# Performance work log

Measured on AMD Instinct MI355X. Metric: run time of the kernel, lower is better.

The kernel has to match this reference:

```python
import jax, jax.numpy as jnp
import numpy as np

D_MODEL = 256; N_HEADS = 8; N_LEVELS = 4; N_POINTS = 4; D_FF = 2048
SHAPES = [(128, 128), (64, 64), (32, 32), (16, 16)]  # (H_l, W_l) per level
LV = sum(h * w for h, w in SHAPES)  # 21760
B = 8; NQ = 900
EPS = 1e-5


def layer_norm(x, s, b):
    m = x.mean(-1, keepdims=True)
    v = x.var(-1, keepdims=True)
    return (x - m) * jax.lax.rsqrt(v + EPS) * s + b


def mha(q, k, v, in_w, in_b, out_w, out_b):
    # torch nn.MultiheadAttention, batch_first, eval mode (no dropout)
    Bq, Lq, C = q.shape
    h = N_HEADS; d = C // h
    wq, wk, wv = jnp.split(in_w, 3, axis=0)
    bq, bk, bv = jnp.split(in_b, 3)
    qh = (q @ wq.T + bq).reshape(Bq, Lq, h, d)
    kh = (k @ wk.T + bk).reshape(Bq, -1, h, d)
    vh = (v @ wv.T + bv).reshape(Bq, -1, h, d)
    scale = jnp.asarray(1.0 / np.sqrt(d), q.dtype)
    attn = jax.nn.softmax(jnp.einsum('bqhd,bkhd->bhqk', qh, kh) * scale, axis=-1)
    o = jnp.einsum('bhqk,bkhd->bqhd', attn, vh).reshape(Bq, Lq, C)
    return o @ out_w.T + out_b


def deform_attn(query, ref, memory, spatial_shapes, val_w, val_b, off_w, off_b, aw_w, aw_b, co_w, co_b):
    # MSDeformAttn forward (eval): offsets/weights from query, bilinear sample value per level/point
    Bq, Lq, C = query.shape
    h, L, P = N_HEADS, N_LEVELS, N_POINTS
    dh = C // h
    value = (memory @ val_w.T + val_b).reshape(Bq, -1, h, dh)  # (B, Lv, h, dh)
    off = (query @ off_w.T + off_b).reshape(Bq, Lq, h, L, P, 2)
    aw = jax.nn.softmax((query @ aw_w.T + aw_b).reshape(Bq, Lq, h, L * P), axis=-1)
    aw = aw.reshape(Bq, Lq, h, L, P)
    # normalizer = (W_l, H_l) per level
    normalizer = spatial_shapes[:, ::-1].astype(query.dtype)
    loc = ref[:, :, None, :, None, :] + off / normalizer[None, None, None, :, None, :]  # (B,Lq,h,L,P,2)
    out = jnp.zeros((Bq, h, Lq, dh), query.dtype)
    start = 0
    for l, (Hl, Wl) in enumerate(SHAPES):
        v_l = value[:, start:start + Hl * Wl].transpose(0, 2, 1, 3)  # (B,h,Hl*Wl,dh)
        start += Hl * Wl
        xy = loc[:, :, :, l]  # (B,Lq,h,P,2) normalized in [0,1]
        # grid_sample align_corners=False pixel coords
        x = xy[..., 0] * Wl - 0.5
        y = xy[..., 1] * Hl - 0.5
        x0 = jnp.floor(x); y0 = jnp.floor(y)
        wx = x - x0; wy = y - y0
        acc = jnp.zeros((Bq, h, Lq * P, dh), query.dtype)
        for dx, dy, w in ((0, 0, (1 - wx) * (1 - wy)), (1, 0, wx * (1 - wy)),
                          (0, 1, (1 - wx) * wy), (1, 1, wx * wy)):
            xi = x0 + dx; yi = y0 + dy
            valid = (xi >= 0) & (xi <= Wl - 1) & (yi >= 0) & (yi <= Hl - 1)
            xi = jnp.clip(xi, 0, Wl - 1).astype(jnp.int32)
            yi = jnp.clip(yi, 0, Hl - 1).astype(jnp.int32)
            idx = (yi * Wl + xi).transpose(0, 2, 1, 3).reshape(Bq, h, Lq * P)
            g = jnp.take_along_axis(v_l, idx[..., None], axis=2)  # (B,h,Lq*P,dh)
            wgt = (w * valid).transpose(0, 2, 1, 3).reshape(Bq, h, Lq * P)
            acc = acc + g * wgt[..., None]
        acc = acc.reshape(Bq, h, Lq, P, dh)
        wl = aw[:, :, :, l].transpose(0, 2, 1, 3)  # (B,h,Lq,P)
        out = out + jnp.einsum('bhqpd,bhqp->bhqd', acc, wl)
    out = out.transpose(0, 2, 1, 3).reshape(Bq, Lq, C)
    return out @ co_w.T + co_b


def forward(tgt, memory, query_pos, reference_points, sa_in_w, sa_in_b, sa_out_w, sa_out_b,
            off_w, off_b, aw_w, aw_b, val_w, val_b, co_w, co_b,
            l1_w, l1_b, l2_w, l2_b, ln1_s, ln1_b, ln2_s, ln2_b, ln3_s, ln3_b, spatial_shapes):
    q = tgt + query_pos  # with_pos_embed; eval mode: no group_detr split, no dropout
    tgt2 = mha(q, q, tgt, sa_in_w, sa_in_b, sa_out_w, sa_out_b)
    tgt = layer_norm(tgt + tgt2, ln1_s, ln1_b)
    tgt2 = deform_attn(tgt + query_pos, reference_points, memory, spatial_shapes,
                       val_w, val_b, off_w, off_b, aw_w, aw_b, co_w, co_b)
    tgt = layer_norm(tgt + tgt2, ln2_s, ln2_b)
    tgt2 = jax.nn.relu(tgt @ l1_w.T + l1_b) @ l2_w.T + l2_b
    return layer_norm(tgt + tgt2, ln3_s, ln3_b)


def setup_inputs():
    key = jax.random.key(0)
    ks = jax.random.split(key, 16)
    C = D_MODEL
    f = lambda i, shape, s=0.02: jax.random.normal(ks[i], shape, jnp.float32) * s
    HLP = N_HEADS * N_LEVELS * N_POINTS
    return {
        'tgt': f(0, (B, NQ, C), 1.0),
        'memory': f(1, (B, LV, C), 1.0),
        'query_pos': f(2, (B, NQ, C), 1.0),
        'reference_points': jax.random.uniform(ks[3], (B, NQ, N_LEVELS, 2), jnp.float32),
        'sa_in_w': f(4, (3 * C, C)), 'sa_in_b': jnp.zeros((3 * C,), jnp.float32),
        'sa_out_w': f(5, (C, C)), 'sa_out_b': jnp.zeros((C,), jnp.float32),
        'off_w': f(6, (HLP * 2, C)), 'off_b': f(7, (HLP * 2,), 0.5),
        'aw_w': f(8, (HLP, C)), 'aw_b': jnp.zeros((HLP,), jnp.float32),
        'val_w': f(9, (C, C)), 'val_b': jnp.zeros((C,), jnp.float32),
        'co_w': f(10, (C, C)), 'co_b': jnp.zeros((C,), jnp.float32),
        'l1_w': f(11, (D_FF, C)), 'l1_b': jnp.zeros((D_FF,), jnp.float32),
        'l2_w': f(12, (C, D_FF)), 'l2_b': jnp.zeros((C,), jnp.float32),
        'ln1_s': jnp.ones((C,), jnp.float32), 'ln1_b': jnp.zeros((C,), jnp.float32),
        'ln2_s': jnp.ones((C,), jnp.float32), 'ln2_b': jnp.zeros((C,), jnp.float32),
        'ln3_s': jnp.ones((C,), jnp.float32), 'ln3_b': jnp.zeros((C,), jnp.float32),
        'spatial_shapes': jnp.asarray(SHAPES, jnp.int32),
        'level_start_index': jnp.asarray(np.cumsum([0] + [h * w for h, w in SHAPES[:-1]]), jnp.int32),
    }


def reference(tgt, memory, query_pos, reference_points, sa_in_w, sa_in_b, sa_out_w, sa_out_b,
              off_w, off_b, aw_w, aw_b, val_w, val_b, co_w, co_b,
              l1_w, l1_b, l2_w, l2_b, ln1_s, ln1_b, ln2_s, ln2_b, ln3_s, ln3_b,
              spatial_shapes, level_start_index):
    return forward(tgt, memory, query_pos, reference_points, sa_in_w, sa_in_b, sa_out_w, sa_out_b,
                   off_w, off_b, aw_w, aw_b, val_w, val_b, co_w, co_b,
                   l1_w, l1_b, l2_w, l2_b, ln1_s, ln1_b, ln2_s, ln2_b, ln3_s, ln3_b, spatial_shapes)
```

## Files before the change

### kernel.cpp

```cpp
#include <hip/hip_runtime.h>
#include <hip/hip_bf16.h>

#define NQL 900
#define CDIM 256
#define BDIM 8
#define LVTOT 21760

typedef __bf16 bf16x8 __attribute__((ext_vector_type(8)));
typedef float f32x4 __attribute__((ext_vector_type(4)));
typedef uint u32x4 __attribute__((ext_vector_type(4)));
typedef uint u32x2 __attribute__((ext_vector_type(2)));

__device__ __forceinline__ ushort f2bf(float x) {
  uint u = __builtin_bit_cast(uint, x);
  u += 0x7fff + ((u >> 16) & 1);
  return (ushort)(u >> 16);
}

template <bool ABF16, bool AADD, bool RELU, bool OUTBF16>
__global__ __launch_bounds__(256, 4) void mgemm_kernel(const void* __restrict__ Ap,
                                                       const float* __restrict__ A2p,
                                                       const float* __restrict__ W,
                                                       const float* __restrict__ bias,
                                                       void* __restrict__ Cout,
                                                       int M, int N, int K) {
  __shared__ ushort smem[10240];
  ushort* As = smem;
  ushort* Bs = smem + 5120;
  const int tid = threadIdx.x;
  const int m0 = blockIdx.y * 128, n0 = blockIdx.x * 128;
  const int wv = tid >> 6;
  const int wm = (wv >> 1) * 64, wn = (wv & 1) * 64;
  const int lane = tid & 63;
  const int lr = lane & 15, kq = lane >> 4;

  f32x4 acc[4][4] = {};
  float4 pa[2][2], pb[2][2];
  u32x4 pa16[2];

  auto load_tiles = [&](int k0) {
#pragma unroll
    for (int it = 0; it < 2; ++it) {
      int idx = it * 256 + tid;
      int r = idx >> 2, s = (idx & 3) << 3;
      int gm = min(m0 + r, M - 1);
      if constexpr (ABF16) {
        pa16[it] = *(const u32x4*)((const ushort*)Ap + (size_t)gm * K + k0 + s);
      } else {
        const float* ap = (const float*)Ap + (size_t)gm * K + k0 + s;
        pa[it][0] = *(const float4*)ap;
        pa[it][1] = *(const float4*)(ap + 4);
        if constexpr (AADD) {
          const float* ap2 = A2p + (size_t)gm * K + k0 + s;
          float4 q0 = *(const float4*)ap2;
          float4 q1 = *(const float4*)(ap2 + 4);
          pa[it][0].x += q0.x; pa[it][0].y += q0.y; pa[it][0].z += q0.z; pa[it][0].w += q0.w;
          pa[it][1].x += q1.x; pa[it][1].y += q1.y; pa[it][1].z += q1.z; pa[it][1].w += q1.w;
        }
      }
      int gn = min(n0 + r, N - 1);
      const float* wp = W + (size_t)gn * K + k0 + s;
      pb[it][0] = *(const float4*)wp;
      pb[it][1] = *(const float4*)(wp + 4);
    }
  };

  auto store_tiles = [&]() {
#pragma unroll
    for (int it = 0; it < 2; ++it) {
      int idx = it * 256 + tid;
      int r = idx >> 2, s = (idx & 3) << 3;
      u32x4 u;
      if constexpr (ABF16) {
        u = pa16[it];
      } else {
        u.x = f2bf(pa[it][0].x) | ((uint)f2bf(pa[it][0].y) << 16);
        u.y = f2bf(pa[it][0].z) | ((uint)f2bf(pa[it][0].w) << 16);
        u.z = f2bf(pa[it][1].x) | ((uint)f2bf(pa[it][1].y) << 16);
        u.w = f2bf(pa[it][1].z) | ((uint)f2bf(pa[it][1].w) << 16);
      }
      *(u32x4*)&As[r * 40 + s] = u;
      u32x4 w;
      w.x = f2bf(pb[it][0].x) | ((uint)f2bf(pb[it][0].y) << 16);
      w.y = f2bf(pb[it][0].z) | ((uint)f2bf(pb[it][0].w) << 16);
      w.z = f2bf(pb[it][1].x) | ((uint)f2bf(pb[it][1].y) << 16);
      w.w = f2bf(pb[it][1].z) | ((uint)f2bf(pb[it][1].w) << 16);
      *(u32x4*)&Bs[r * 40 + s] = w;
    }
  };

  load_tiles(0);
  for (int k0 = 0; k0 < K; k0 += 32) {
    store_tiles();
    __syncthreads();
    if (k0 + 32 < K) load_tiles(k0 + 32);
    bf16x8 af[4], bq[4];
#pragma unroll
    for (int m = 0; m < 4; ++m)
      af[m] = __builtin_bit_cast(bf16x8, *(const u32x4*)&As[(wm + m * 16 + lr) * 40 + kq * 8]);
#pragma unroll
    for (int n = 0; n < 4; ++n)
      bq[n] = __builtin_bit_cast(bf16x8, *(const u32x4*)&Bs[(wn + n * 16 + lr) * 40 + kq * 8]);
#pragma unroll
    for (int m = 0; m < 4; ++m)
#pragma unroll
      for (int n = 0; n < 4; ++n)
        acc[m][n] = __builtin_amdgcn_mfma_f32_16x16x32_bf16(af[m], bq[n], acc[m][n], 0, 0, 0);
    __syncthreads();
  }

  if constexpr (OUTBF16) {
    ushort* Cs = smem;
#pragma unroll
    for (int p = 0; p < 2; ++p) {
      __syncthreads();
      if (wm == p * 64) {
#pragma unroll
        for (int n = 0; n < 4; ++n) {
          int col = wn + n * 16 + lr;
          float bv = bias[n0 + col];
#pragma unroll
          for (int m = 0; m < 4; ++m)
#pragma unroll
            for (int j = 0; j < 4; ++j) {
              float v = acc[m][n][j] + bv;
              if (RELU) v = fmaxf(v, 0.f);
              Cs[(m * 16 + kq * 4 + j) * 136 + col] = f2bf(v);
            }
        }
      }
      __syncthreads();
#pragma unroll
      for (int it = 0; it < 4; ++it) {
        int idx = it * 256 + tid;
        int r = idx >> 4, c = (idx & 15) * 8;
        int grow = m0 + p * 64 + r;
        if (grow < M) {
          u32x4 u = *(const u32x4*)&Cs[r * 136 + c];
          *(u32x4*)((ushort*)Cout + (size_t)grow * N + n0 + c) = u;
        }
      }
    }
  } else {
#pragma unroll
    for (int n = 0; n < 4; ++n) {
      int gcol = n0 + wn + n * 16 + lr;
      float bv = bias[gcol];
#pragma unroll
      for (int m = 0; m < 4; ++m) {
        int rbase = m0 + wm + m * 16 + kq * 4;
#pragma unroll
        for (int j = 0; j < 4; ++j) {
          int grow = rbase + j;
          if (grow >= M) continue;
          float v = acc[m][n][j] + bv;
          if (RELU) v = fmaxf(v, 0.f);
          ((float*)Cout)[(size_t)grow * N + gcol] = v;
        }
      }
    }
  }
}

template <bool ABF16, bool AADD, bool RELU, bool HASRES, bool DOSM, bool OUTBF16>
__global__ __launch_bounds__(256, 4) void mgemm64_kernel(const void* __restrict__ Ap,
                                                         const float* __restrict__ A2p,
                                                         const float* __restrict__ W,
                                                         const float* __restrict__ bias,
                                                         const float* __restrict__ Rres,
                                                         void* __restrict__ Cout,
                                                         int M, int N, int K) {
  __shared__ ushort smem[5120];
  ushort* As = smem;
  ushort* Bs = smem + 2560;
  const int tid = threadIdx.x;
  const int m0 = blockIdx.y * 64, n0 = blockIdx.x * 64;
  const int wv = tid >> 6, lane = tid & 63;
  const int wm = (wv >> 1) * 32, wn = (wv & 1) * 32;
  const int lr = lane & 15, kq = lane >> 4;

  f32x4 acc[2][2] = {};
  float4 pa[2], pb[2];
  u32x4 pa16;

  auto load_tiles = [&](int k0) {
    int r = tid >> 2, s = (tid & 3) << 3;
    int gm = min(m0 + r, M - 1);
    if constexpr (ABF16) {
      pa16 = *(const u32x4*)((const ushort*)Ap + (size_t)gm * K + k0 + s);
    } else {
      const float* ap = (const float*)Ap + (size_t)gm * K + k0 + s;
      pa[0] = *(const float4*)ap;
      pa[1] = *(const float4*)(ap + 4);
      if constexpr (AADD) {
        const float* ap2 = A2p + (size_t)gm * K + k0 + s;
        float4 q0 = *(const float4*)ap2;
        float4 q1 = *(const float4*)(ap2 + 4);
        pa[0].x += q0.x; pa[0].y += q0.y; pa[0].z += q0.z; pa[0].w += q0.w;
        pa[1].x += q1.x; pa[1].y += q1.y; pa[1].z += q1.z; pa[1].w += q1.w;
      }
    }
    int gn = min(n0 + r, N - 1);
    const float* wp = W + (size_t)gn * K + k0 + s;
    pb[0] = *(const float4*)wp;
    pb[1] = *(const float4*)(wp + 4);
  };

  auto store_tiles = [&]() {
    int r = tid >> 2, s = (tid & 3) << 3;
    u32x4 u;
    if constexpr (ABF16) {
      u = pa16;
    } else {
      u.x = f2bf(pa[0].x) | ((uint)f2bf(pa[0].y) << 16);
      u.y = f2bf(pa[0].z) | ((uint)f2bf(pa[0].w) << 16);
      u.z = f2bf(pa[1].x) | ((uint)f2bf(pa[1].y) << 16);
      u.w = f2bf(pa[1].z) | ((uint)f2bf(pa[1].w) << 16);
    }
    *(u32x4*)&As[r * 40 + s] = u;
    u32x4 w;
    w.x = f2bf(pb[0].x) | ((uint)f2bf(pb[0].y) << 16);
    w.y = f2bf(pb[0].z) | ((uint)f2bf(pb[0].w) << 16);
    w.z = f2bf(pb[1].x) | ((uint)f2bf(pb[1].y) << 16);
    w.w = f2bf(pb[1].z) | ((uint)f2bf(pb[1].w) << 16);
    *(u32x4*)&Bs[r * 40 + s] = w;
  };

  load_tiles(0);
  for (int k0 = 0; k0 < K; k0 += 32) {
    store_tiles();
    __syncthreads();
    if (k0 + 32 < K) load_tiles(k0 + 32);
    bf16x8 af[2], bq[2];
#pragma unroll
    for (int m = 0; m < 2; ++m)
      af[m] = __builtin_bit_cast(bf16x8, *(const u32x4*)&As[(wm + m * 16 + lr) * 40 + kq * 8]);
#pragma unroll
    for (int n = 0; n < 2; ++n)
      bq[n] = __builtin_bit_cast(bf16x8, *(const u32x4*)&Bs[(wn + n * 16 + lr) * 40 + kq * 8]);
#pragma unroll
    for (int m = 0; m < 2; ++m)
#pragma unroll
      for (int n = 0; n < 2; ++n)
        acc[m][n] = __builtin_amdgcn_mfma_f32_16x16x32_bf16(af[m], bq[n], acc[m][n], 0, 0, 0);
    __syncthreads();
  }

  if constexpr (OUTBF16) {
    ushort* Cs = smem;
    __syncthreads();
#pragma unroll
    for (int n = 0; n < 2; ++n) {
      int col = wn + n * 16 + lr;
      float bv = bias[n0 + col];
#pragma unroll
      for (int m = 0; m < 2; ++m)
#pragma unroll
        for (int j = 0; j < 4; ++j) {
          float v = acc[m][n][j] + bv;
          if (RELU) v = fmaxf(v, 0.f);
          Cs[(wm + m * 16 + kq * 4 + j) * 72 + col] = f2bf(v);
        }
    }
    __syncthreads();
#pragma unroll
    for (int it = 0; it < 2; ++it) {
      int idx = it * 256 + tid;
      int r = idx >> 3, c = (idx & 7) * 8;
      int grow = m0 + r;
      if (grow < M) {
        u32x4 u = *(const u32x4*)&Cs[r * 72 + c];
        *(u32x4*)((ushort*)Cout + (size_t)grow * N + n0 + c) = u;
      }
    }
  } else {
#pragma unroll
    for (int n = 0; n < 2; ++n) {
      int gcol = n0 + wn + n * 16 + lr;
      float bv = bias[gcol];
#pragma unroll
      for (int m = 0; m < 2; ++m) {
        int rbase = m0 + wm + m * 16 + kq * 4;
#pragma unroll
        for (int j = 0; j < 4; ++j) {
          int grow = rbase + j;
          float v = acc[m][n][j] + bv;
          if constexpr (DOSM) {
            float gmax = v;
#pragma unroll
            for (int w = 1; w < 16; w <<= 1) gmax = fmaxf(gmax, __shfl_xor(gmax, w));
            float e = __expf(v - gmax);
            float gs = e;
#pragma unroll
            for (int w = 1; w < 16; w <<= 1) gs += __shfl_xor(gs, w);
            v = e / gs;
          }
          if (grow >= M) continue;
          if (HASRES) v += Rres[(size_t)grow * N + gcol];
          if (RELU) v = fmaxf(v, 0.f);
          ((float*)Cout)[(size_t)grow * N + gcol] = v;
        }
      }
    }
  }
}

template <bool ABF16, bool OUTBF16>
__global__ __launch_bounds__(256, 4) void mgemm256_kernel(const void* __restrict__ Ap,
                                                          const float* __restrict__ W,
                                                          const float* __restrict__ bias,
                                                          void* __restrict__ Cout,
                                                          int M, int K) {
  __shared__ ushort smem[12800];
  ushort* As = smem;
  ushort* Bs = smem + 2560;
  const int tid = threadIdx.x;
  const int m0 = blockIdx.x * 64;
  const int wv = tid >> 6;
  const int lane = tid & 63;
  const int lr = lane & 15, kq = lane >> 4;

  f32x4 acc[16] = {};
  float4 pa[2];
  u32x4 pa16;
  float4 pb[4][2];

  auto load_tiles = [&](int k0) {
    {
      int r = tid >> 2, s = (tid & 3) << 3;
      int gm = min(m0 + r, M - 1);
      if constexpr (ABF16) {
        pa16 = *(const u32x4*)((const ushort*)Ap + (size_t)gm * K + k0 + s);
      } else {
        const float* ap = (const float*)Ap + (size_t)gm * K + k0 + s;
        pa[0] = *(const float4*)ap;
        pa[1] = *(const float4*)(ap + 4);
      }
    }
#pragma unroll
    for (int it = 0; it < 4; ++it) {
      int idx = it * 256 + tid;
      int r = idx >> 2, s = (idx & 3) << 3;
      const float* wp = W + (size_t)r * K + k0 + s;
      pb[it][0] = *(const float4*)wp;
      pb[it][1] = *(const float4*)(wp + 4);
    }
  };

  auto store_tiles = [&]() {
    {
      int r = tid >> 2, s = (tid & 3) << 3;
      u32x4 u;
      if constexpr (ABF16) {
        u = pa16;
      } else {
        u.x = f2bf(pa[0].x) | ((uint)f2bf(pa[0].y) << 16);
        u.y = f2bf(pa[0].z) | ((uint)f2bf(pa[0].w) << 16);
        u.z = f2bf(pa[1].x) | ((uint)f2bf(pa[1].y) << 16);
        u.w = f2bf(pa[1].z) | ((uint)f2bf(pa[1].w) << 16);
      }
      *(u32x4*)&As[r * 40 + s] = u;
    }
#pragma unroll
    for (int it = 0; it < 4; ++it) {
      int idx = it * 256 + tid;
      int r = idx >> 2, s = (idx & 3) << 3;
      u32x4 w;
      w.x = f2bf(pb[it][0].x) | ((uint)f2bf(pb[it][0].y) << 16);
      w.y = f2bf(pb[it][0].z) | ((uint)f2bf(pb[it][0].w) << 16);
      w.z = f2bf(pb[it][1].x) | ((uint)f2bf(pb[it][1].y) << 16);
      w.w = f2bf(pb[it][1].z) | ((uint)f2bf(pb[it][1].w) << 16);
      *(u32x4*)&Bs[r * 40 + s] = w;
    }
  };

  load_tiles(0);
  for (int k0 = 0; k0 < K; k0 += 32) {
    store_tiles();
    __syncthreads();
    if (k0 + 32 < K) load_tiles(k0 + 32);
    bf16x8 af = __builtin_bit_cast(bf16x8, *(const u32x4*)&As[(wv * 16 + lr) * 40 + kq * 8]);
#pragma unroll
    for (int ng = 0; ng < 16; ++ng) {
      bf16x8 bq = __builtin_bit_cast(bf16x8, *(const u32x4*)&Bs[(ng * 16 + lr) * 40 + kq * 8]);
      acc[ng] = __builtin_amdgcn_mfma_f32_16x16x32_bf16(af, bq, acc[ng], 0, 0, 0);
    }
    __syncthreads();
  }

  if constexpr (OUTBF16) {
    ushort* Cs = smem;
#pragma unroll
    for (int p = 0; p < 2; ++p) {
      __syncthreads();
      if ((wv >> 1) == p) {
#pragma unroll
        for (int nf = 0; nf < 16; ++nf) {
          int col = nf * 16 + lr;
          float bv = bias[col];
#pragma unroll
          for (int j = 0; j < 4; ++j) {
            int row = (wv & 1) * 16 + kq * 4 + j;
            Cs[row * 264 + col] = f2bf(acc[nf][j] + bv);
          }
        }
      }
      __syncthreads();
#pragma unroll
      for (int it = 0; it < 4; ++it) {
        int idx = it * 256 + tid;
        int r = idx >> 5, c = (idx & 31) * 8;
        int grow = m0 + p * 32 + r;
        if (grow < M) {
          u32x4 u = *(const u32x4*)&Cs[r * 264 + c];
          *(u32x4*)((ushort*)Cout + (size_t)grow * 256 + c) = u;
        }
      }
    }
  } else {
#pragma unroll
    for (int nf = 0; nf < 16; ++nf) {
      int col = nf * 16 + lr;
      float bv = bias[col];
#pragma unroll
      for (int j = 0; j < 4; ++j) {
        int grow = m0 + wv * 16 + kq * 4 + j;
        if (grow < M)
          ((float*)Cout)[(size_t)grow * 256 + col] = acc[nf][j] + bv;
      }
    }
  }
}

__global__ __launch_bounds__(256) void vt_kernel(const ushort* __restrict__ tmp_v,
                                                 ushort* __restrict__ vt) {
  __shared__ ushort Ls[64 * 40];
  const int qt = blockIdx.x;
  const int bh = blockIdx.y;
  const int b = bh >> 3, h = bh & 7;
  const int tid = threadIdx.x;
  const int q0 = qt * 64;
  {
    int r = tid >> 2, c = (tid & 3) * 8;
    int gq = min(q0 + r, NQL - 1);
    u32x4 u = *(const u32x4*)(tmp_v + ((size_t)(b * NQL + gq) * 256) + h * 32 + c);
    *(u32x4*)&Ls[r * 40 + c] = u;
  }
  __syncthreads();
  {
    int d = tid >> 3, qw = (tid & 7) * 8;
    u32x4 u;
    uint w[8];
#pragma unroll
    for (int j = 0; j < 8; ++j) w[j] = Ls[(qw + j) * 40 + d];
    u.x = w[0] | (w[1] << 16);
    u.y = w[2] | (w[3] << 16);
    u.z = w[4] | (w[5] << 16);
    u.w = w[6] | (w[7] << 16);
    *(u32x4*)(vt + ((size_t)(bh * 32 + d) * 960) + q0 + qw) = u;
  }
}

__global__ __launch_bounds__(256, 2) void fattn_kernel(const ushort* __restrict__ qk,
                                                       const ushort* __restrict__ vt,
                                                       float* __restrict__ out) {
  __shared__ ushort Ks[64 * 40];
  __shared__ ushort Vs[32 * 72];
  __shared__ ushort Ps[4][16 * 72];
  const int qt = blockIdx.x, bh = blockIdx.y;
  const int b = bh >> 3, h = bh & 7;
  const int tid = threadIdx.x;
  const int wv = tid >> 6, lane = tid & 63;
  const int lq = lane & 15, hi = lane >> 4;
  const int q0 = qt * 64 + wv * 16;
  const float SC = 0.17677669529663689f;

  bf16x8 qfrag;
  {
    int qrow = min(q0 + lq, NQL - 1);
    qfrag = __builtin_bit_cast(bf16x8,
        *(const u32x4*)(qk + (size_t)(b * NQL + qrow) * 512 + h * 32 + hi * 8));
  }

  f32x4 o0 = {}, o1 = {};
  float mrow = -1e30f, lrow = 0.f;

  for (int kt = 0; kt < 15; ++kt) {
    const int k0 = kt * 64;
    __syncthreads();
    {
      int r = tid >> 2, c = (tid & 3) * 8;
      int gk = min(k0 + r, NQL - 1);
      u32x4 u = *(const u32x4*)(qk + (size_t)(b * NQL + gk) * 512 + 256 + h * 32 + c);
      *(u32x4*)&Ks[r * 40 + c] = u;
    }
    {
      int r = tid >> 3, c = (tid & 7) * 8;
      u32x4 u = *(const u32x4*)(vt + (size_t)(bh * 32 + r) * 960 + k0 + c);
      *(u32x4*)&Vs[r * 72 + c] = u;
    }
    __syncthreads();

    f32x4 st[4];
#pragma unroll
    for (int mt = 0; mt < 4; ++mt) {
      bf16x8 kf = __builtin_bit_cast(bf16x8, *(const u32x4*)&Ks[(mt * 16 + lq) * 40 + hi * 8]);
      f32x4 z = {};
      st[mt] = __builtin_amdgcn_mfma_f32_16x16x32_bf16(kf, qfrag, z, 0, 0, 0);
    }
    float sv[4][4];
    float lmax = -1e30f;
#pragma unroll
    for (int mt = 0; mt < 4; ++mt)
#pragma unroll
      for (int j = 0; j < 4; ++j) {
        int key = k0 + mt * 16 + hi * 4 + j;
        float v = st[mt][j] * SC;
        v = (key < NQL) ? v : -1e30f;
        sv[mt][j] = v;
        lmax = fmaxf(lmax, v);
      }
    lmax = fmaxf(lmax, __shfl_xor(lmax, 16));
    lmax = fmaxf(lmax, __shfl_xor(lmax, 32));
    float mnew = fmaxf(mrow, lmax);
    float rs = __expf(mrow - mnew);
    float lsum = 0.f;
    uint pw[4][2];
#pragma unroll
    for (int mt = 0; mt < 4; ++mt) {
      float p0 = __expf(sv[mt][0] - mnew);
      float p1 = __expf(sv[mt][1] - mnew);
      float p2 = __expf(sv[mt][2] - mnew);
      float p3 = __expf(sv[mt][3] - mnew);
      lsum += (p0 + p1) + (p2 + p3);
      pw[mt][0] = f2bf(p0) | ((uint)f2bf(p1) << 16);
      pw[mt][1] = f2bf(p2) | ((uint)f2bf(p3) << 16);
    }
    lsum += __shfl_xor(lsum, 16);
    lsum += __shfl_xor(lsum, 32);
    lrow = lrow * rs + lsum;
    mrow = mnew;
#pragma unroll
    for (int j = 0; j < 4; ++j) {
      float rsj = __shfl(rs, hi * 4 + j);
      o0[j] *= rsj;
      o1[j] *= rsj;
    }
#pragma unroll
    for (int mt = 0; mt < 4; ++mt) {
      u32x2 u;
      u.x = pw[mt][0];
      u.y = pw[mt][1];
      *(u32x2*)&Ps[wv][lq * 72 + mt * 16 + hi * 4] = u;
    }
#pragma unroll
    for (int k2 = 0; k2 < 2; ++k2) {
      bf16x8 pa = __builtin_bit_cast(bf16x8, *(const u32x4*)&Ps[wv][lq * 72 + k2 * 32 + hi * 8]);
      bf16x8 vb0 = __builtin_bit_cast(bf16x8, *(const u32x4*)&Vs[(0 * 16 + lq) * 72 + k2 * 32 + hi * 8]);
      bf16x8 vb1 = __builtin_bit_cast(bf16x8, *(const u32x4*)&Vs[(1 * 16 + lq) * 72 + k2 * 32 + hi * 8]);
      o0 = __builtin_amdgcn_mfma_f32_16x16x32_bf16(pa, vb0, o0, 0, 0, 0);
      o1 = __builtin_amdgcn_mfma_f32_16x16x32_bf16(pa, vb1, o1, 0, 0, 0);
    }
  }

#pragma unroll
  for (int j = 0; j < 4; ++j) {
    float lj = __shfl(lrow, hi * 4 + j);
    float inv = 1.f / lj;
    int gq = q0 + hi * 4 + j;
    if (gq < NQL) {
      float* op = out + (size_t)(b * NQL + gq) * 256 + h * 32;
      op[lq] = o0[j] * inv;
      op[16 + lq] = o1[j] * inv;
    }
  }
}

__global__ __launch_bounds__(256) void ln_kernel(const float* __restrict__ x,
                                                 const float* __restrict__ s,
                                                 const float* __restrict__ bb,
                                                 float* __restrict__ out, int M) {
  const int wv = threadIdx.x >> 6, lane = threadIdx.x & 63;
  const int row = blockIdx.x * 4 + wv;
  if (row >= M) return;
  const float4 v = *(const float4*)(x + (size_t)row * 256 + lane * 4);
  float s1 = (v.x + v.y) + (v.z + v.w);
  float s2 = (v.x * v.x + v.y * v.y) + (v.z * v.z + v.w * v.w);
#pragma unroll
  for (int w = 1; w < 64; w <<= 1) {
    s1 += __shfl_xor(s1, w);
    s2 += __shfl_xor(s2, w);
  }
  float mean = s1 * (1.f / 256.f);
  float var = s2 * (1.f / 256.f) - mean * mean;
  float inv = rsqrtf(var + 1e-5f);
  float4 sc = *(const float4*)(s + lane * 4);
  float4 bv = *(const float4*)(bb + lane * 4);
  float4 o;
  o.x = (v.x - mean) * inv * sc.x + bv.x;
  o.y = (v.y - mean) * inv * sc.y + bv.y;
  o.z = (v.z - mean) * inv * sc.z + bv.z;
  o.w = (v.w - mean) * inv * sc.w + bv.w;
  *(float4*)(out + (size_t)row * 256 + lane * 4) = o;
}

__global__ __launch_bounds__(256) void deform_kernel(const __hip_bfloat16* __restrict__ value,
                                                     const float* __restrict__ offb,
                                                     const float* __restrict__ awb,
                                                     const float* __restrict__ refp,
                                                     float* __restrict__ dfout) {
  const int Hs[4] = {128, 64, 32, 16};
  const int Stl[4] = {0, 16384, 20480, 21504};
  int row = blockIdx.x;
  int b = row / NQL;
  int tid = threadIdx.x;
  int h = tid >> 5, d = tid & 31;
  const float* off = offb + (size_t)row * 256;
  const float* aw = awb + (size_t)row * 128;
  const float* ref = refp + (size_t)row * 8;
  const __hip_bfloat16* vb = value + (size_t)b * LVTOT * 256 + h * 32 + d;
  float acc = 0.f;
#pragma unroll
  for (int l = 0; l < 4; ++l) {
    int Wi = Hs[l], Hi = Hs[l];
    float Wl = (float)Wi, Hl = (float)Hi;
    int st = Stl[l];
    float rx = ref[l * 2 + 0], ry = ref[l * 2 + 1];
#pragma unroll
    for (int p = 0; p < 4; ++p) {
      int oi = ((h * 4 + l) * 4 + p) * 2;
      float x = (rx + off[oi] / Wl) * Wl - 0.5f;
      float y = (ry + off[oi + 1] / Hl) * Hl - 0.5f;
      float w = aw[h * 16 + l * 4 + p];
      float x0f = floorf(x), y0f = floorf(y);
      float wx = x - x0f, wy = y - y0f;
      int xi0 = (int)x0f, yi0 = (int)y0f;
      float samp = 0.f;
#pragma unroll
      for (int dy = 0; dy < 2; ++dy) {
#pragma unroll
        for (int dx = 0; dx < 2; ++dx) {
          int xi = xi0 + dx, yi = yi0 + dy;
          float tw = (dx ? wx : 1.f - wx) * (dy ? wy : 1.f - wy);
          bool valid = (xi >= 0) && (xi < Wi) && (yi >= 0) && (yi < Hi);
          int xc = min(max(xi, 0), Wi - 1);
          int yc = min(max(yi, 0), Hi - 1);
          float vv = __bfloat162float(vb[(size_t)(st + yc * Wi + xc) * 256]);
          samp += valid ? tw * vv : 0.f;
        }
      }
      acc = fmaf(w, samp, acc);
    }
  }
  dfout[(size_t)row * 256 + tid] = acc;
}

extern "C" void kernel_launch(void* const* d_in, const int* in_sizes, int n_in,
                              void* d_out, int out_size, void* d_ws, size_t ws_size,
                              hipStream_t stream) {
  const float* tgt = (const float*)d_in[0];
  const float* memory = (const float*)d_in[1];
  const float* qpos = (const float*)d_in[2];
  const float* refp = (const float*)d_in[3];
  const float* sa_in_w = (const float*)d_in[4];
  const float* sa_in_b = (const float*)d_in[5];
  const float* sa_out_w = (const float*)d_in[6];
  const float* sa_out_b = (const float*)d_in[7];
  const float* off_w = (const float*)d_in[8];
  const float* off_b = (const float*)d_in[9];
  const float* aw_w = (const float*)d_in[10];
  const float* aw_b = (const float*)d_in[11];
  const float* val_w = (const float*)d_in[12];
  const float* val_b = (const float*)d_in[13];
  const float* co_w = (const float*)d_in[14];
  const float* co_b = (const float*)d_in[15];
  const float* l1_w = (const float*)d_in[16];
  const float* l1_b = (const float*)d_in[17];
  const float* l2_w = (const float*)d_in[18];
  const float* l2_b = (const float*)d_in[19];
  const float* ln1_s = (const float*)d_in[20];
  const float* ln1_b = (const float*)d_in[21];
  const float* ln2_s = (const float*)d_in[22];
  const float* ln2_b = (const float*)d_in[23];
  const float* ln3_s = (const float*)d_in[24];
  const float* ln3_b = (const float*)d_in[25];

  float* ws = (float*)d_ws;
  const size_t E = (size_t)BDIM * NQL * CDIM;
  ushort* vt = (ushort*)(ws + E);
  float* attn_o = ws + 4 * E;
  ushort* tmp_qk = (ushort*)(ws + 5 * E);
  ushort* tmp_v = (ushort*)(ws + 7 * E);
  float* sa_out = ws + 5 * E;
  float* offb = ws + E;
  float* awb = ws + 2 * E;
  float* dfout = ws + 3 * E;
  float* co_out = ws + 4 * E;
  ushort* hidden = (ushort*)ws;
  float* ffn_o = ws + 4 * E;
  float* tgt1 = ws + 8 * E;
  float* tgt2 = ws + 9 * E;
  ushort* valbf = (ushort*)(ws + 11 * E);

  const int M = BDIM * NQL;
  const int MT = (M + 127) / 128;
  const int M64 = (M + 63) / 64;
  const int LNG = (M + 3) / 4;
  dim3 blk(256);

  mgemm64_kernel<false, true, false, false, false, true><<<dim3(8, M64), blk, 0, stream>>>(
      tgt, qpos, sa_in_w, sa_in_b, nullptr, tmp_qk, M, 512, 256);
  mgemm64_kernel<false, false, false, false, false, true><<<dim3(4, M64), blk, 0, stream>>>(
      tgt, nullptr, sa_in_w + 512 * 256, sa_in_b + 512, nullptr, tmp_v, M, 256, 256);
  vt_kernel<<<dim3(15, 64), blk, 0, stream>>>(tmp_v, vt);
  fattn_kernel<<<dim3(15, 64), blk, 0, stream>>>(tmp_qk, vt, attn_o);
  mgemm64_kernel<false, false, false, true, false, false><<<dim3(4, M64), blk, 0, stream>>>(
      attn_o, nullptr, sa_out_w, sa_out_b, tgt, sa_out, M, 256, 256);
  ln_kernel<<<LNG, blk, 0, stream>>>(sa_out, ln1_s, ln1_b, tgt1, M);
  mgemm256_kernel<false, true><<<(BDIM * LVTOT) / 64, blk, 0, stream>>>(
      memory, val_w, val_b, valbf, BDIM * LVTOT, 256);
  mgemm64_kernel<false, true, false, false, false, false><<<dim3(4, M64), blk, 0, stream>>>(
      tgt1, qpos, off_w, off_b, nullptr, offb, M, 256, 256);
  mgemm64_kernel<false, true, false, false, true, false><<<dim3(2, M64), blk, 0, stream>>>(
      tgt1, qpos, aw_w, aw_b, nullptr, awb, M, 128, 256);
  deform_kernel<<<M, blk, 0, stream>>>((const __hip_bfloat16*)valbf, offb, awb, refp, dfout);
  mgemm64_kernel<false, false, false, true, false, false><<<dim3(4, M64), blk, 0, stream>>>(
      dfout, nullptr, co_w, co_b, tgt1, co_out, M, 256, 256);
  ln_kernel<<<LNG, blk, 0, stream>>>(co_out, ln2_s, ln2_b, tgt2, M);
  mgemm_kernel<false, false, true, true><<<dim3(16, MT), blk, 0, stream>>>(
      tgt2, nullptr, l1_w, l1_b, hidden, M, 2048, 256);
  mgemm64_kernel<true, false, false, true, false, false><<<dim3(4, M64), blk, 0, stream>>>(
      hidden, nullptr, l2_w, l2_b, tgt2, ffn_o, M, 256, 2048);
  ln_kernel<<<LNG, blk, 0, stream>>>(ffn_o, ln3_s, ln3_b, (float*)d_out, M);
}
```

Measured before the change: 359.4 us.

## Pre-convert value weights to bf16 and stage full A row-tile in LDS

Adds a small kernel that converts the value-projection weight to bf16 once per call, and rewrites the value projection GEMM to load the whole 64x256 fp32 memory tile up front into LDS as bf16. Per k-step it now only streams pre-converted bf16 weights instead of reloading and converting fp32 weights in every block. This removes the repeated per-block fp32-to-bf16 conversion of W and halves weight traffic. The cost is a larger LDS footprint (lower occupancy, launch bounds 2) and one extra small launch.

Result: no change. 357.3 us (-0.6%).

```diff
diff --git a/kernel.cpp b/kernel.cpp
--- a/kernel.cpp
+++ b/kernel.cpp
@@ -305,81 +305,65 @@
   }
 }
 
-template <bool ABF16, bool OUTBF16>
-__global__ __launch_bounds__(256, 4) void mgemm256_kernel(const void* __restrict__ Ap,
-                                                          const float* __restrict__ W,
-                                                          const float* __restrict__ bias,
-                                                          void* __restrict__ Cout,
-                                                          int M, int K) {
-  __shared__ ushort smem[12800];
-  ushort* As = smem;
-  ushort* Bs = smem + 2560;
+__global__ __launch_bounds__(256) void wconv_kernel(const float* __restrict__ W,
+                                                    ushort* __restrict__ Wbf) {
+  int idx = (blockIdx.x * 256 + threadIdx.x) * 4;
+  float4 v = *(const float4*)(W + idx);
+  u32x2 u;
+  u.x = f2bf(v.x) | ((uint)f2bf(v.y) << 16);
+  u.y = f2bf(v.z) | ((uint)f2bf(v.w) << 16);
+  *(u32x2*)(Wbf + idx) = u;
+}
+
+__global__ __launch_bounds__(256, 2) void vproj_kernel(const float* __restrict__ A,
+                                                       const ushort* __restrict__ Wbf,
+                                                       const float* __restrict__ bias,
+                                                       ushort* __restrict__ Cout) {
+  __shared__ ushort As[64 * 264];
+  __shared__ ushort Bs[256 * 40];
   const int tid = threadIdx.x;
   const int m0 = blockIdx.x * 64;
-  const int wv = tid >> 6;
-  const int lane = tid & 63;
+  const int wv = tid >> 6, lane = tid & 63;
   const int lr = lane & 15, kq = lane >> 4;
 
+  {
+    const float* base = A + (size_t)m0 * 256;
+    float4 v[16];
+#pragma unroll
+    for (int it = 0; it < 16; ++it)
+      v[it] = *(const float4*)(base + (size_t)(it * 256 + tid) * 4);
+#pragma unroll
+    for (int it = 0; it < 16; ++it) {
+      int f4 = it * 256 + tid;
+      int row = f4 >> 6;
+      int col = (f4 & 63) * 4;
+      u32x2 w;
+      w.x = f2bf(v[it].x) | ((uint)f2bf(v[it].y) << 16);
+      w.y = f2bf(v[it].z) | ((uint)f2bf(v[it].w) << 16);
+      *(u32x2*)&As[row * 264 + col] = w;
+    }
+  }
+
+  u32x4 pw[4];
+  auto loadW = [&](int k0) {
+#pragma unroll
+    for (int i = 0; i < 4; ++i)
+      pw[i] = *(const u32x4*)(Wbf + (size_t)tid * 256 + k0 + i * 8);
+  };
+  auto storeW = [&]() {
+#pragma unroll
+    for (int i = 0; i < 4; ++i)
+      *(u32x4*)&Bs[tid * 40 + i * 8] = pw[i];
+  };
+
   f32x4 acc[16] = {};
-  float4 pa[2];
-  u32x4 pa16;
-  float4 pb[4][2];
-
-  auto load_tiles = [&](int k0) {
-    {
-      int r = tid >> 2, s = (tid & 3) << 3;
-      int gm = min(m0 + r, M - 1);
-      if constexpr (ABF16) {
-        pa16 = *(const u32x4*)((const ushort*)Ap + (size_t)gm * K + k0 + s);
-      } else {
-        const float* ap = (const float*)Ap + (size_t)gm * K + k0 + s;
-        pa[0] = *(const float4*)ap;
-        pa[1] = *(const float4*)(ap + 4);
-      }
-    }
-#pragma unroll
-    for (int it = 0; it < 4; ++it) {
-      int idx = it * 256 + tid;
-      int r = idx >> 2, s = (idx & 3) << 3;
-      const float* wp = W + (size_t)r * K + k0 + s;
-      pb[it][0] = *(const float4*)wp;
-      pb[it][1] = *(const float4*)(wp + 4);
-    }
-  };
-
-  auto store_tiles = [&]() {
-    {
-      int r = tid >> 2, s = (tid & 3) << 3;
-      u32x4 u;
-      if constexpr (ABF16) {
-        u = pa16;
-      } else {
-        u.x = f2bf(pa[0].x) | ((uint)f2bf(pa[0].y) << 16);
-        u.y = f2bf(pa[0].z) | ((uint)f2bf(pa[0].w) << 16);
-        u.z = f2bf(pa[1].x) | ((uint)f2bf(pa[1].y) << 16);
-        u.w = f2bf(pa[1].z) | ((uint)f2bf(pa[1].w) << 16);
-      }
-      *(u32x4*)&As[r * 40 + s] = u;
-    }
-#pragma unroll
-    for (int it = 0; it < 4; ++it) {
-      int idx = it * 256 + tid;
-      int r = idx >> 2, s = (idx & 3) << 3;
-      u32x4 w;
-      w.x = f2bf(pb[it][0].x) | ((uint)f2bf(pb[it][0].y) << 16);
-      w.y = f2bf(pb[it][0].z) | ((uint)f2bf(pb[it][0].w) << 16);
-      w.z = f2bf(pb[it][1].x) | ((uint)f2bf(pb[it][1].y) << 16);
-      w.w = f2bf(pb[it][1].z) | ((uint)f2bf(pb[it][1].w) << 16);
-      *(u32x4*)&Bs[r * 40 + s] = w;
-    }
-  };
-
-  load_tiles(0);
-  for (int k0 = 0; k0 < K; k0 += 32) {
-    store_tiles();
-    __syncthreads();
-    if (k0 + 32 < K) load_tiles(k0 + 32);
-    bf16x8 af = __builtin_bit_cast(bf16x8, *(const u32x4*)&As[(wv * 16 + lr) * 40 + kq * 8]);
+  loadW(0);
+  for (int k0 = 0; k0 < 256; k0 += 32) {
+    storeW();
+    __syncthreads();
+    if (k0 + 32 < 256) loadW(k0 + 32);
+    bf16x8 af = __builtin_bit_cast(bf16x8,
+        *(const u32x4*)&As[(wv * 16 + lr) * 264 + k0 + kq * 8]);
 #pragma unroll
     for (int ng = 0; ng < 16; ++ng) {
       bf16x8 bq = __builtin_bit_cast(bf16x8, *(const u32x4*)&Bs[(ng * 16 + lr) * 40 + kq * 8]);
@@ -388,47 +372,24 @@
     __syncthreads();
   }
 
-  if constexpr (OUTBF16) {
-    ushort* Cs = smem;
-#pragma unroll
-    for (int p = 0; p < 2; ++p) {
-      __syncthreads();
-      if ((wv >> 1) == p) {
-#pragma unroll
-        for (int nf = 0; nf < 16; ++nf) {
-          int col = nf * 16 + lr;
-          float bv = bias[col];
-#pragma unroll
-          for (int j = 0; j < 4; ++j) {
-            int row = (wv & 1) * 16 + kq * 4 + j;
-            Cs[row * 264 + col] = f2bf(acc[nf][j] + bv);
-          }
-        }
-      }
-      __syncthreads();
-#pragma unroll
-      for (int it = 0; it < 4; ++it) {
-        int idx = it * 256 + tid;
-        int r = idx >> 5, c = (idx & 31) * 8;
-        int grow = m0 + p * 32 + r;
-        if (grow < M) {
-          u32x4 u = *(const u32x4*)&Cs[r * 264 + c];
-          *(u32x4*)((ushort*)Cout + (size_t)grow * 256 + c) = u;
-        }
-      }
-    }
-  } else {
-#pragma unroll
-    for (int nf = 0; nf < 16; ++nf) {
-      int col = nf * 16 + lr;
-      float bv = bias[col];
-#pragma unroll
-      for (int j = 0; j < 4; ++j) {
-        int grow = m0 + wv * 16 + kq * 4 + j;
-        if (grow < M)
-          ((float*)Cout)[(size_t)grow * 256 + col] = acc[nf][j] + bv;
-      }
-    }
+  ushort* Cs = As;
+#pragma unroll
+  for (int nf = 0; nf < 16; ++nf) {
+    int col = nf * 16 + lr;
+    float bv = bias[col];
+#pragma unroll
+    for (int j = 0; j < 4; ++j) {
+      int row = wv * 16 + kq * 4 + j;
+      Cs[row * 264 + col] = f2bf(acc[nf][j] + bv);
+    }
+  }
+  __syncthreads();
+#pragma unroll
+  for (int it = 0; it < 8; ++it) {
+    int idx = it * 256 + tid;
+    int r = idx >> 5, c = (idx & 31) * 8;
+    u32x4 u = *(const u32x4*)&Cs[r * 264 + c];
+    *(u32x4*)(Cout + (size_t)(m0 + r) * 256 + c) = u;
   }
 }
 
@@ -700,6 +661,7 @@
   float* ffn_o = ws + 4 * E;
   float* tgt1 = ws + 8 * E;
   float* tgt2 = ws + 9 * E;
+  ushort* wbf = (ushort*)(ws + 10 * E);
   ushort* valbf = (ushort*)(ws + 11 * E);
 
   const int M = BDIM * NQL;
@@ -708,6 +670,7 @@
   const int LNG = (M + 3) / 4;
   dim3 blk(256);
 
+  wconv_kernel<<<64, blk, 0, stream>>>(val_w, wbf);
   mgemm64_kernel<false, true, false, false, false, true><<<dim3(8, M64), blk, 0, stream>>>(
       tgt, qpos, sa_in_w, sa_in_b, nullptr, tmp_qk, M, 512, 256);
   mgemm64_kernel<false, false, false, false, false, true><<<dim3(4, M64), blk, 0, stream>>>(
@@ -717,8 +680,7 @@
   mgemm64_kernel<false, false, false, true, false, false><<<dim3(4, M64), blk, 0, stream>>>(
       attn_o, nullptr, sa_out_w, sa_out_b, tgt, sa_out, M, 256, 256);
   ln_kernel<<<LNG, blk, 0, stream>>>(sa_out, ln1_s, ln1_b, tgt1, M);
-  mgemm256_kernel<false, true><<<(BDIM * LVTOT) / 64, blk, 0, stream>>>(
-      memory, val_w, val_b, valbf, BDIM * LVTOT, 256);
+  vproj_kernel<<<(BDIM * LVTOT) / 64, blk, 0, stream>>>(memory, wbf, val_b, valbf);
   mgemm64_kernel<false, true, false, false, false, false><<<dim3(4, M64), blk, 0, stream>>>(
       tgt1, qpos, off_w, off_b, nullptr, offb, M, 256, 256);
   mgemm64_kernel<false, true, false, false, true, false><<<dim3(2, M64), blk, 0, stream>>>(
```
